# Kernel tuning notes

Measured on AMD Instinct MI355X. Metric: run time of the kernel, lower is better.

The kernel has to match this reference:

```python
import jax, jax.numpy as jnp
import numpy as np

N_NODES = 50000
N_EDGES = 600000
D = 128
N_GRAPHS = 64


def setup_inputs() -> dict:
    key = jax.random.key(0)
    ks = jax.random.split(key, 16)
    x = jax.random.normal(ks[0], (N_NODES, D), dtype=jnp.float32)
    edge_index = jax.random.randint(ks[1], (2, N_EDGES), 0, N_NODES, dtype=jnp.int64)
    batch = jnp.sort(jax.random.randint(ks[2], (N_NODES,), 0, N_GRAPHS, dtype=jnp.int64))
    s = 1.0 / np.sqrt(D)
    def lin(k, out_d, in_d):
        return jax.random.uniform(k, (out_d, in_d), jnp.float32, -s, s)
    inp = {"x": x, "edge_index": edge_index, "batch": batch}
    for i, base in zip(range(3), (3, 6, 9)):
        inp[f"W_rel{i+1}"] = lin(ks[base], D, D)
        inp[f"b_rel{i+1}"] = jax.random.uniform(ks[base + 1], (D,), jnp.float32, -s, s)
        inp[f"W_root{i+1}"] = lin(ks[base + 2], D, D)
    s5 = 1.0 / np.sqrt(5)
    inp["W1"] = lin(ks[12], 5, D)
    inp["b1"] = jax.random.uniform(ks[13], (5,), jnp.float32, -s, s)
    inp["W2"] = jax.random.uniform(ks[14], (1, 5), jnp.float32, -s5, s5)
    inp["b2"] = jax.random.uniform(ks[15], (1,), jnp.float32, -s5, s5)
    return inp


def graph_conv(x, src, dst, W_rel, b_rel, W_root):
    # PyG GraphConv: out_i = W_root x_i + W_rel * sum_{j->i} x_j + b_rel
    agg = jax.ops.segment_sum(x[src], dst, num_segments=N_NODES)  # [N, D]
    return agg @ W_rel.T + b_rel + x @ W_root.T


def reference(x, edge_index, batch,
              W_rel1, b_rel1, W_root1,
              W_rel2, b_rel2, W_root2,
              W_rel3, b_rel3, W_root3,
              W1, b1, W2, b2):
    src, dst = edge_index[0], edge_index[1]
    h = jax.nn.relu(graph_conv(x, src, dst, W_rel1, b_rel1, W_root1))
    h = jax.nn.relu(graph_conv(h, src, dst, W_rel2, b_rel2, W_root2))
    h = graph_conv(h, src, dst, W_rel3, b_rel3, W_root3)
    # global max pool over graphs
    g = jax.ops.segment_max(h, batch, num_segments=N_GRAPHS)  # [G, D]
    out = jax.nn.relu(g @ W1.T + b1) @ W2.T + b2  # [G, 1]
    return out
```

## Files before the change

kernel.cpp:

```cpp
#include <hip/hip_runtime.h>
#include <float.h>

#define N_NODES 50000
#define N_EDGES 600000
#define D 128
#define N_GRAPHS 64
#define SCAN_T 256
#define SCAN_NBLK ((N_NODES + SCAN_T - 1) / SCAN_T)

typedef __attribute__((ext_vector_type(8))) short short8;
typedef __attribute__((ext_vector_type(4))) float floatx4;

__device__ inline float bf2f(unsigned short h) {
    return __uint_as_float((unsigned)h << 16);
}
__device__ inline unsigned short f2bf(float f) {
    unsigned u = __float_as_uint(f);
    return (unsigned short)((u + 0x7fffu + ((u >> 16) & 1u)) >> 16);
}


__global__ void cast_prep(const float4* __restrict__ x,
                          ushort4* __restrict__ xb0, ushort4* __restrict__ xb1, int n4,
                          const float* __restrict__ Wr0, const float* __restrict__ Wo0,
                          const float* __restrict__ Wr1, const float* __restrict__ Wo1,
                          const float* __restrict__ Wr2, const float* __restrict__ Wo2,
                          unsigned short* __restrict__ B0, unsigned short* __restrict__ B1,
                          unsigned short* __restrict__ B2,
                          int* __restrict__ deg, float* __restrict__ g) {
    int idx = blockIdx.x * 256 + threadIdx.x;
    if (idx < N_NODES) deg[idx] = 0;
    if (idx < N_GRAPHS * D) g[idx] = -FLT_MAX;
    if (idx < n4) {
        float4 v = x[idx];
        ushort4 o;
        o.x = f2bf(v.x); o.y = f2bf(v.y); o.z = f2bf(v.z); o.w = f2bf(v.w);
        int node = idx >> 5;
        int q    = idx & 31;
        ushort4* dst = (q < 16) ? xb0 : xb1;
        dst[(size_t)node * 16 + (q & 15)] = o;
        return;
    }
    int w = idx - n4;
    if (w >= 3 * 128 * 256) return;
    int l = w >> 15;
    int r = w & 32767;
    int o = r >> 8, k = r & 255;
    const float* Wr = (l == 0) ? Wr0 : (l == 1) ? Wr1 : Wr2;
    const float* Wo = (l == 0) ? Wo0 : (l == 1) ? Wo1 : Wo2;
    unsigned short* B = (l == 0) ? B0 : (l == 1) ? B1 : B2;
    float v = (k < 128) ? Wr[o * 128 + k] : Wo[o * 128 + (k - 128)];
    B[r] = f2bf(v);
}


__global__ void count_deg(const int* __restrict__ ei, int* __restrict__ deg) {
    int e = blockIdx.x * 256 + threadIdx.x;
    if (e < N_EDGES) atomicAdd(&deg[ei[N_EDGES + e]], 1);
}

__global__ __launch_bounds__(SCAN_T) void block_sum(const int* __restrict__ deg,
                                                    int* __restrict__ blockSums) {
    __shared__ int s[SCAN_T];
    int tid = threadIdx.x;
    int i = blockIdx.x * SCAN_T + tid;
    s[tid] = (i < N_NODES) ? deg[i] : 0;
    __syncthreads();
    for (int off = SCAN_T / 2; off > 0; off >>= 1) {
        if (tid < off) s[tid] += s[tid + off];
        __syncthreads();
    }
    if (tid == 0) blockSums[blockIdx.x] = s[0];
}

__global__ __launch_bounds__(SCAN_T) void scan_write(const int* __restrict__ deg,
                                                     const int* __restrict__ blockSums,
                                                     int* __restrict__ row_start,
                                                     int* __restrict__ cursor) {
    __shared__ int bs[SCAN_T];
    __shared__ int s[SCAN_T];
    int tid = threadIdx.x;
    bs[tid] = (tid < SCAN_NBLK) ? blockSums[tid] : 0;
    __syncthreads();
    for (int off = 1; off < SCAN_T; off <<= 1) {
        int t = (tid >= off) ? bs[tid - off] : 0;
        __syncthreads();
        bs[tid] += t;
        __syncthreads();
    }
    int myOff = (blockIdx.x == 0) ? 0 : bs[blockIdx.x - 1];
    if (blockIdx.x == 0 && tid == SCAN_T - 1) row_start[N_NODES] = bs[tid];

    int i = blockIdx.x * SCAN_T + tid;
    int v = (i < N_NODES) ? deg[i] : 0;
    s[tid] = v;
    __syncthreads();
    for (int off = 1; off < SCAN_T; off <<= 1) {
        int t = (tid >= off) ? s[tid - off] : 0;
        __syncthreads();
        s[tid] += t;
        __syncthreads();
    }
    if (i < N_NODES) {
        int rs = myOff + s[tid] - v;
        row_start[i] = rs;
        cursor[i]    = rs;
    }
}

__global__ void fill_csr(const int* __restrict__ ei, int* __restrict__ cursor,
                         int* __restrict__ csr_src) {
    int e = blockIdx.x * 256 + threadIdx.x;
    if (e < N_EDGES) {
        int dst = ei[N_EDGES + e];
        int pos = atomicAdd(&cursor[dst], 1);
        csr_src[pos] = ei[e];
    }
}


#define ACC8(u) { a[0] += bf2f((unsigned short)(u)[0]); a[1] += bf2f((unsigned short)(u)[1]); \
                  a[2] += bf2f((unsigned short)(u)[2]); a[3] += bf2f((unsigned short)(u)[3]); \
                  a[4] += bf2f((unsigned short)(u)[4]); a[5] += bf2f((unsigned short)(u)[5]); \
                  a[6] += bf2f((unsigned short)(u)[6]); a[7] += bf2f((unsigned short)(u)[7]); }

__global__ __launch_bounds__(256) void gather_half(
    const unsigned short* __restrict__ xh,
    const int* __restrict__ row_start, const int* __restrict__ csr_src,
    unsigned short* __restrict__ aggh)
{
    int grp  = threadIdx.x >> 3;
    int ln   = threadIdx.x & 7;
    int node = blockIdx.x * 32 + grp;
    if (node >= N_NODES) return;
    int beg = row_start[node];
    int end = row_start[node + 1];

    float a[8];
#pragma unroll
    for (int i = 0; i < 8; ++i) a[i] = 0.f;

    for (int base = beg; base < end; base += 8) {
        int n = end - base; if (n > 8) n = 8;
        int idx = (ln < n) ? csr_src[base + ln] : 0;
        int j = 0;
        for (; j + 7 < n; j += 8) {
            int s0 = __shfl(idx, 0, 8); int s1 = __shfl(idx, 1, 8);
            int s2 = __shfl(idx, 2, 8); int s3 = __shfl(idx, 3, 8);
            int s4 = __shfl(idx, 4, 8); int s5 = __shfl(idx, 5, 8);
            int s6 = __shfl(idx, 6, 8); int s7 = __shfl(idx, 7, 8);
            short8 u0 = *(const short8*)(xh + (size_t)s0 * 64 + ln * 8);
            short8 u1 = *(const short8*)(xh + (size_t)s1 * 64 + ln * 8);
            short8 u2 = *(const short8*)(xh + (size_t)s2 * 64 + ln * 8);
            short8 u3 = *(const short8*)(xh + (size_t)s3 * 64 + ln * 8);
            short8 u4 = *(const short8*)(xh + (size_t)s4 * 64 + ln * 8);
            short8 u5 = *(const short8*)(xh + (size_t)s5 * 64 + ln * 8);
            short8 u6 = *(const short8*)(xh + (size_t)s6 * 64 + ln * 8);
            short8 u7 = *(const short8*)(xh + (size_t)s7 * 64 + ln * 8);
            ACC8(u0); ACC8(u1); ACC8(u2); ACC8(u3);
            ACC8(u4); ACC8(u5); ACC8(u6); ACC8(u7);
        }
        for (; j + 3 < n; j += 4) {
            int s0 = __shfl(idx, j,     8); int s1 = __shfl(idx, j + 1, 8);
            int s2 = __shfl(idx, j + 2, 8); int s3 = __shfl(idx, j + 3, 8);
            short8 u0 = *(const short8*)(xh + (size_t)s0 * 64 + ln * 8);
            short8 u1 = *(const short8*)(xh + (size_t)s1 * 64 + ln * 8);
            short8 u2 = *(const short8*)(xh + (size_t)s2 * 64 + ln * 8);
            short8 u3 = *(const short8*)(xh + (size_t)s3 * 64 + ln * 8);
            ACC8(u0); ACC8(u1); ACC8(u2); ACC8(u3);
        }
        for (; j < n; ++j) {
            int s0 = __shfl(idx, j, 8);
            short8 u0 = *(const short8*)(xh + (size_t)s0 * 64 + ln * 8);
            ACC8(u0);
        }
    }
    short8 r;
#pragma unroll
    for (int i = 0; i < 8; ++i) r[i] = (short)f2bf(a[i]);
    *(short8*)(aggh + (size_t)node * 64 + ln * 8) = r;
}


__device__ inline void stage_b_half(unsigned short* sB, const unsigned short* __restrict__ Bb,
                                    int tid, int h) {
#pragma unroll
    for (int i = 0; i < 8; ++i) {
        int flat = tid + i * 256;
        int fi = flat >> 6, ln = flat & 63;
        int mm = ln & 15, qq = ln >> 4;
        int ksL = fi >> 3, tt = fi & 7;
        short8 v = *(const short8*)(Bb + (size_t)(tt * 16 + mm) * 256
                                    + (h * 4 + ksL) * 32 + qq * 8);
        *(short8*)(sB + (size_t)flat * 8) = v;
    }
}


__global__ __launch_bounds__(256) void gemm_mfma(
    const unsigned short* __restrict__ agg0, const unsigned short* __restrict__ agg1,
    const unsigned short* __restrict__ x0,   const unsigned short* __restrict__ x1,
    const unsigned short* __restrict__ Bb, const float* __restrict__ bias,
    unsigned short* __restrict__ O0, unsigned short* __restrict__ O1, int relu)
{
    __shared__ unsigned short sB[16384];
    int tid  = threadIdx.x;
    int wave = tid >> 6;
    int lane = tid & 63;
    int m    = lane & 15;
    int quad = lane >> 4;
    int row0 = blockIdx.x * 64 + wave * 16;

    int arow = row0 + m;
    if (arow > N_NODES - 1) arow = N_NODES - 1;

    short8 af[8];
#pragma unroll
    for (int ks = 0; ks < 8; ++ks) {
        const unsigned short* Asrc =
            (ks < 2) ? agg0 : (ks < 4) ? agg1 : (ks < 6) ? x0 : x1;
        af[ks] = *(const short8*)(Asrc + (size_t)arow * 64 + (ks & 1) * 32 + quad * 8);
    }

    floatx4 acc[8];
#pragma unroll
    for (int t = 0; t < 8; ++t) acc[t] = (floatx4){0.f, 0.f, 0.f, 0.f};

    stage_b_half(sB, Bb, tid, 0);
    __syncthreads();
#pragma unroll
    for (int ksL = 0; ksL < 4; ++ksL)
#pragma unroll
        for (int t = 0; t < 8; ++t) {
            short8 b = *(const short8*)(sB + (size_t)((ksL * 8 + t) * 64 + lane) * 8);
            acc[t] = __builtin_amdgcn_mfma_f32_16x16x32_bf16(af[ksL], b, acc[t], 0, 0, 0);
        }
    __syncthreads();
    stage_b_half(sB, Bb, tid, 1);
    __syncthreads();
#pragma unroll
    for (int ksL = 0; ksL < 4; ++ksL)
#pragma unroll
        for (int t = 0; t < 8; ++t) {
            short8 b = *(const short8*)(sB + (size_t)((ksL * 8 + t) * 64 + lane) * 8);
            acc[t] = __builtin_amdgcn_mfma_f32_16x16x32_bf16(af[4 + ksL], b, acc[t], 0, 0, 0);
        }

#pragma unroll
    for (int t = 0; t < 8; ++t) {
        int col = t * 16 + m;
        float bv = bias[col];
        unsigned short* Oh = (t < 4) ? O0 : O1;
#pragma unroll
        for (int r = 0; r < 4; ++r) {
            int row = row0 + quad * 4 + r;
            if (row >= N_NODES) continue;
            float v = acc[t][r] + bv;
            if (relu) v = fmaxf(v, 0.f);
            Oh[(size_t)row * 64 + (col & 63)] = f2bf(v);
        }
    }
}


struct PoolShared {
    union {
        unsigned short b[16384];
        float c[64 * 129];
    };
};

__global__ __launch_bounds__(256) void gemm_pool(
    const unsigned short* __restrict__ agg0, const unsigned short* __restrict__ agg1,
    const unsigned short* __restrict__ x0,   const unsigned short* __restrict__ x1,
    const unsigned short* __restrict__ Bb, const float* __restrict__ bias,
    const int* __restrict__ batch, float* __restrict__ g)
{
    __shared__ PoolShared sh;
    __shared__ int bl[64];
    int tid  = threadIdx.x;
    int wave = tid >> 6;
    int lane = tid & 63;
    int m    = lane & 15;
    int quad = lane >> 4;
    int row0 = blockIdx.x * 64;

    int arow = row0 + wave * 16 + m;
    if (arow > N_NODES - 1) arow = N_NODES - 1;

    short8 af[8];
#pragma unroll
    for (int ks = 0; ks < 8; ++ks) {
        const unsigned short* Asrc =
            (ks < 2) ? agg0 : (ks < 4) ? agg1 : (ks < 6) ? x0 : x1;
        af[ks] = *(const short8*)(Asrc + (size_t)arow * 64 + (ks & 1) * 32 + quad * 8);
    }

    floatx4 acc[8];
#pragma unroll
    for (int t = 0; t < 8; ++t) acc[t] = (floatx4){0.f, 0.f, 0.f, 0.f};

    if (tid < 64) {
        int grow = row0 + tid;
        bl[tid] = (grow < N_NODES) ? batch[grow] : -1;
    }
    stage_b_half(sh.b, Bb, tid, 0);
    __syncthreads();
#pragma unroll
    for (int ksL = 0; ksL < 4; ++ksL)
#pragma unroll
        for (int t = 0; t < 8; ++t) {
            short8 b = *(const short8*)(sh.b + (size_t)((ksL * 8 + t) * 64 + lane) * 8);
            acc[t] = __builtin_amdgcn_mfma_f32_16x16x32_bf16(af[ksL], b, acc[t], 0, 0, 0);
        }
    __syncthreads();
    stage_b_half(sh.b, Bb, tid, 1);
    __syncthreads();
#pragma unroll
    for (int ksL = 0; ksL < 4; ++ksL)
#pragma unroll
        for (int t = 0; t < 8; ++t) {
            short8 b = *(const short8*)(sh.b + (size_t)((ksL * 8 + t) * 64 + lane) * 8);
            acc[t] = __builtin_amdgcn_mfma_f32_16x16x32_bf16(af[4 + ksL], b, acc[t], 0, 0, 0);
        }
    __syncthreads();

#pragma unroll
    for (int t = 0; t < 8; ++t) {
        int col = t * 16 + m;
        float bv = bias[col];
#pragma unroll
        for (int r = 0; r < 4; ++r)
            sh.c[(wave * 16 + quad * 4 + r) * 129 + col] = acc[t][r] + bv;
    }
    __syncthreads();

    int nvalid = min(64, N_NODES - row0);
    int b0 = bl[0], b1 = bl[nvalid - 1];
    int col  = tid & 127;
    int rbeg = (tid >> 7) * 32;
    for (int gg = b0; gg <= b1; ++gg) {
        float cur = -FLT_MAX;
#pragma unroll
        for (int r = 0; r < 32; ++r) {
            int rr = rbeg + r;
            float v = (bl[rr] == gg) ? sh.c[rr * 129 + col] : -FLT_MAX;
            cur = fmaxf(cur, v);
        }
        if (cur > -FLT_MAX) {
            float* ad = &g[gg * D + col];
            if (cur >= 0.f) atomicMax((int*)ad, __float_as_int(cur));
            else            atomicMin((unsigned int*)ad, __float_as_uint(cur));
        }
    }
}


__global__ __launch_bounds__(64) void mlp_head(const float* __restrict__ g,
                         const float* __restrict__ W1, const float* __restrict__ b1,
                         const float* __restrict__ W2, const float* __restrict__ b2,
                         float* __restrict__ out) {
    int gi = blockIdx.x;
    int lane = threadIdx.x;
    float x0 = g[gi * D + lane];
    float x1 = g[gi * D + 64 + lane];
    float o = b2[0];
#pragma unroll
    for (int j = 0; j < 5; ++j) {
        float p = x0 * W1[j * D + lane] + x1 * W1[j * D + 64 + lane];
#pragma unroll
        for (int off = 32; off > 0; off >>= 1) p += __shfl_xor(p, off, 64);
        o += fmaxf(p + b1[j], 0.f) * W2[j];
    }
    if (lane == 0) out[gi] = o;
}

extern "C" void kernel_launch(void* const* d_in, const int* in_sizes, int n_in,
                              void* d_out, int out_size, void* d_ws, size_t ws_size,
                              hipStream_t stream) {
    const float* x     = (const float*)d_in[0];
    const int*   ei    = (const int*)d_in[1];
    const int*   batch = (const int*)d_in[2];
    const float* Wrel[3]  = {(const float*)d_in[3], (const float*)d_in[6], (const float*)d_in[9]};
    const float* brel[3]  = {(const float*)d_in[4], (const float*)d_in[7], (const float*)d_in[10]};
    const float* Wroot[3] = {(const float*)d_in[5], (const float*)d_in[8], (const float*)d_in[11]};
    const float* W1 = (const float*)d_in[12];
    const float* b1 = (const float*)d_in[13];
    const float* W2 = (const float*)d_in[14];
    const float* b2 = (const float*)d_in[15];
    float* out = (float*)d_out;

    char* ws = (char*)d_ws;
    const size_t halfB = (size_t)N_NODES * 64 * sizeof(unsigned short);
    unsigned short* xb0  = (unsigned short*)(ws);
    unsigned short* xb1  = (unsigned short*)(ws + 1 * halfB);
    unsigned short* hb10 = (unsigned short*)(ws + 2 * halfB);
    unsigned short* hb11 = (unsigned short*)(ws + 3 * halfB);
    unsigned short* hb20 = (unsigned short*)(ws + 4 * halfB);
    unsigned short* hb21 = (unsigned short*)(ws + 5 * halfB);
    unsigned short* ag0  = (unsigned short*)(ws + 6 * halfB);
    unsigned short* ag1  = (unsigned short*)(ws + 7 * halfB);
    char* p = ws + 8 * halfB;
    unsigned short* Bb0 = (unsigned short*)p;   p += 128 * 256 * sizeof(unsigned short);
    unsigned short* Bb1 = (unsigned short*)p;   p += 128 * 256 * sizeof(unsigned short);
    unsigned short* Bb2 = (unsigned short*)p;   p += 128 * 256 * sizeof(unsigned short);
    float* g        = (float*)p;                p += N_GRAPHS * D * sizeof(float);
    int*   deg      = (int*)p;                  p += N_NODES * sizeof(int);
    int*   row_start= (int*)p;                  p += (N_NODES + 1) * sizeof(int);
    int*   cursor   = (int*)p;                  p += N_NODES * sizeof(int);
    int*   csr_src  = (int*)p;                  p += N_EDGES * sizeof(int);
    int*   blockSums= (int*)p;                  p += SCAN_NBLK * sizeof(int);

    const int n4 = N_NODES * D / 4;
    const int cast_total = n4 + 3 * 128 * 256;
    cast_prep<<<(cast_total + 255) / 256, 256, 0, stream>>>(
        (const float4*)x, (ushort4*)xb0, (ushort4*)xb1, n4,
        Wrel[0], Wroot[0], Wrel[1], Wroot[1], Wrel[2], Wroot[2],
        Bb0, Bb1, Bb2, deg, g);

    count_deg<<<(N_EDGES + 255) / 256, 256, 0, stream>>>(ei, deg);
    block_sum<<<SCAN_NBLK, SCAN_T, 0, stream>>>(deg, blockSums);
    scan_write<<<SCAN_NBLK, SCAN_T, 0, stream>>>(deg, blockSums, row_start, cursor);
    fill_csr<<<(N_EDGES + 255) / 256, 256, 0, stream>>>(ei, cursor, csr_src);

    const int ggrid = (N_NODES + 31) / 32;
    const int mgrid = (N_NODES + 63) / 64;

    gather_half<<<ggrid, 256, 0, stream>>>(xb0, row_start, csr_src, ag0);
    gather_half<<<ggrid, 256, 0, stream>>>(xb1, row_start, csr_src, ag1);
    gemm_mfma<<<mgrid, 256, 0, stream>>>(ag0, ag1, xb0, xb1, Bb0, brel[0], hb10, hb11, 1);
    gather_half<<<ggrid, 256, 0, stream>>>(hb10, row_start, csr_src, ag0);
    gather_half<<<ggrid, 256, 0, stream>>>(hb11, row_start, csr_src, ag1);
    gemm_mfma<<<mgrid, 256, 0, stream>>>(ag0, ag1, hb10, hb11, Bb1, brel[1], hb20, hb21, 1);
    gather_half<<<ggrid, 256, 0, stream>>>(hb20, row_start, csr_src, ag0);
    gather_half<<<ggrid, 256, 0, stream>>>(hb21, row_start, csr_src, ag1);
    gemm_pool<<<mgrid, 256, 0, stream>>>(ag0, ag1, hb20, hb21, Bb2, brel[2], batch, g);

    mlp_head<<<N_GRAPHS, 64, 0, stream>>>(g, W1, b1, W2, b2, out);
}
```

Baseline: 321.8 us.

## Quantize node features to int8 with per-node scale for neighbor gathers

After: 320.4 us. No clear change (-0.4%).

```diff
diff --git a/kernel.cpp b/kernel.cpp
--- a/kernel.cpp
+++ b/kernel.cpp
@@ -19,38 +19,79 @@
     return (unsigned short)((u + 0x7fffu + ((u >> 16) & 1u)) >> 16);
 }
 
-
-__global__ void cast_prep(const float4* __restrict__ x,
-                          ushort4* __restrict__ xb0, ushort4* __restrict__ xb1, int n4,
-                          const float* __restrict__ Wr0, const float* __restrict__ Wo0,
-                          const float* __restrict__ Wr1, const float* __restrict__ Wo1,
-                          const float* __restrict__ Wr2, const float* __restrict__ Wo2,
-                          unsigned short* __restrict__ B0, unsigned short* __restrict__ B1,
-                          unsigned short* __restrict__ B2,
-                          int* __restrict__ deg, float* __restrict__ g) {
-    int idx = blockIdx.x * 256 + threadIdx.x;
-    if (idx < N_NODES) deg[idx] = 0;
-    if (idx < N_GRAPHS * D) g[idx] = -FLT_MAX;
-    if (idx < n4) {
-        float4 v = x[idx];
-        ushort4 o;
-        o.x = f2bf(v.x); o.y = f2bf(v.y); o.z = f2bf(v.z); o.w = f2bf(v.w);
-        int node = idx >> 5;
-        int q    = idx & 31;
-        ushort4* dst = (q < 16) ? xb0 : xb1;
-        dst[(size_t)node * 16 + (q & 15)] = o;
+#define ACCQ(u, ss) {                                                            \
+    int w0_ = (u).x, w1_ = (u).y, w2_ = (u).z, w3_ = (u).w;                      \
+    a[ 0] += (float)(signed char)(w0_      ) * (ss);                             \
+    a[ 1] += (float)(signed char)(w0_ >>  8) * (ss);                             \
+    a[ 2] += (float)(signed char)(w0_ >> 16) * (ss);                             \
+    a[ 3] += (float)(w0_ >> 24)              * (ss);                             \
+    a[ 4] += (float)(signed char)(w1_      ) * (ss);                             \
+    a[ 5] += (float)(signed char)(w1_ >>  8) * (ss);                             \
+    a[ 6] += (float)(signed char)(w1_ >> 16) * (ss);                             \
+    a[ 7] += (float)(w1_ >> 24)              * (ss);                             \
+    a[ 8] += (float)(signed char)(w2_      ) * (ss);                             \
+    a[ 9] += (float)(signed char)(w2_ >>  8) * (ss);                             \
+    a[10] += (float)(signed char)(w2_ >> 16) * (ss);                             \
+    a[11] += (float)(w2_ >> 24)              * (ss);                             \
+    a[12] += (float)(signed char)(w3_      ) * (ss);                             \
+    a[13] += (float)(signed char)(w3_ >>  8) * (ss);                             \
+    a[14] += (float)(signed char)(w3_ >> 16) * (ss);                             \
+    a[15] += (float)(w3_ >> 24)              * (ss); }
+
+
+__global__ __launch_bounds__(256) void cast_prep(
+    const float* __restrict__ x,
+    unsigned short* __restrict__ xb, signed char* __restrict__ xq,
+    float* __restrict__ xs,
+    const float* __restrict__ Wr0, const float* __restrict__ Wo0,
+    const float* __restrict__ Wr1, const float* __restrict__ Wo1,
+    const float* __restrict__ Wr2, const float* __restrict__ Wo2,
+    unsigned short* __restrict__ B0, unsigned short* __restrict__ B1,
+    unsigned short* __restrict__ B2,
+    int* __restrict__ deg, float* __restrict__ g)
+{
+    int t = blockIdx.x * 256 + threadIdx.x;
+    if (t < N_NODES * 16) {
+        int node = t >> 4, ln = t & 15;
+        const float4* xr = (const float4*)(x + (size_t)node * D + ln * 8);
+        float4 v0 = xr[0], v1 = xr[1];
+        float v[8] = {v0.x, v0.y, v0.z, v0.w, v1.x, v1.y, v1.z, v1.w};
+        float am = 0.f;
+#pragma unroll
+        for (int i = 0; i < 8; ++i) am = fmaxf(am, fabsf(v[i]));
+#pragma unroll
+        for (int m = 1; m < 16; m <<= 1) am = fmaxf(am, __shfl_xor(am, m, 16));
+        float inv = (am > 0.f) ? 127.f / am : 0.f;
+        short8 hb;
+#pragma unroll
+        for (int i = 0; i < 8; ++i) hb[i] = (short)f2bf(v[i]);
+        *(short8*)(xb + (size_t)node * D + ln * 8) = hb;
+        int q0 = 0, q1 = 0;
+#pragma unroll
+        for (int i = 0; i < 4; ++i) { int q = (int)rintf(v[i]     * inv); q0 |= (q & 0xff) << (8 * i); }
+#pragma unroll
+        for (int i = 0; i < 4; ++i) { int q = (int)rintf(v[4 + i] * inv); q1 |= (q & 0xff) << (8 * i); }
+        int2 qp; qp.x = q0; qp.y = q1;
+        *(int2*)(xq + (size_t)node * D + ln * 8) = qp;
+        if (ln == 0) xs[node] = am * (1.f / 127.f);
         return;
     }
-    int w = idx - n4;
-    if (w >= 3 * 128 * 256) return;
-    int l = w >> 15;
-    int r = w & 32767;
-    int o = r >> 8, k = r & 255;
-    const float* Wr = (l == 0) ? Wr0 : (l == 1) ? Wr1 : Wr2;
-    const float* Wo = (l == 0) ? Wo0 : (l == 1) ? Wo1 : Wo2;
-    unsigned short* B = (l == 0) ? B0 : (l == 1) ? B1 : B2;
-    float v = (k < 128) ? Wr[o * 128 + k] : Wo[o * 128 + (k - 128)];
-    B[r] = f2bf(v);
+    int w = t - N_NODES * 16;
+    if (w < 3 * 128 * 256) {
+        int l = w >> 15;
+        int r = w & 32767;
+        int o = r >> 8, k = r & 255;
+        const float* Wr = (l == 0) ? Wr0 : (l == 1) ? Wr1 : Wr2;
+        const float* Wo = (l == 0) ? Wo0 : (l == 1) ? Wo1 : Wo2;
+        unsigned short* B = (l == 0) ? B0 : (l == 1) ? B1 : B2;
+        float v = (k < 128) ? Wr[o * 128 + k] : Wo[o * 128 + (k - 128)];
+        B[r] = f2bf(v);
+        return;
+    }
+    w -= 3 * 128 * 256;
+    if (w < N_NODES) { deg[w] = 0; return; }
+    w -= N_NODES;
+    if (w < N_GRAPHS * D) g[w] = -FLT_MAX;
 }
 
 
@@ -83,9 +124,9 @@
     bs[tid] = (tid < SCAN_NBLK) ? blockSums[tid] : 0;
     __syncthreads();
     for (int off = 1; off < SCAN_T; off <<= 1) {
-        int t = (tid >= off) ? bs[tid - off] : 0;
+        int tt = (tid >= off) ? bs[tid - off] : 0;
         __syncthreads();
-        bs[tid] += t;
+        bs[tid] += tt;
         __syncthreads();
     }
     int myOff = (blockIdx.x == 0) ? 0 : bs[blockIdx.x - 1];
@@ -96,9 +137,9 @@
     s[tid] = v;
     __syncthreads();
     for (int off = 1; off < SCAN_T; off <<= 1) {
-        int t = (tid >= off) ? s[tid - off] : 0;
+        int tt = (tid >= off) ? s[tid - off] : 0;
         __syncthreads();
-        s[tid] += t;
+        s[tid] += tt;
         __syncthreads();
     }
     if (i < N_NODES) {
@@ -119,15 +160,10 @@
 }
 
 
-#define ACC8(u) { a[0] += bf2f((unsigned short)(u)[0]); a[1] += bf2f((unsigned short)(u)[1]); \
-                  a[2] += bf2f((unsigned short)(u)[2]); a[3] += bf2f((unsigned short)(u)[3]); \
-                  a[4] += bf2f((unsigned short)(u)[4]); a[5] += bf2f((unsigned short)(u)[5]); \
-                  a[6] += bf2f((unsigned short)(u)[6]); a[7] += bf2f((unsigned short)(u)[7]); }
-
-__global__ __launch_bounds__(256) void gather_half(
-    const unsigned short* __restrict__ xh,
+__global__ __launch_bounds__(256) void gather_q(
+    const signed char* __restrict__ xq, const float* __restrict__ xs,
     const int* __restrict__ row_start, const int* __restrict__ csr_src,
-    unsigned short* __restrict__ aggh)
+    unsigned short* __restrict__ aggb)
 {
     int grp  = threadIdx.x >> 3;
     int ln   = threadIdx.x & 7;
@@ -136,49 +172,36 @@
     int beg = row_start[node];
     int end = row_start[node + 1];
 
-    float a[8];
-#pragma unroll
-    for (int i = 0; i < 8; ++i) a[i] = 0.f;
+    float a[16];
+#pragma unroll
+    for (int i = 0; i < 16; ++i) a[i] = 0.f;
 
     for (int base = beg; base < end; base += 8) {
         int n = end - base; if (n > 8) n = 8;
         int idx = (ln < n) ? csr_src[base + ln] : 0;
         int j = 0;
-        for (; j + 7 < n; j += 8) {
-            int s0 = __shfl(idx, 0, 8); int s1 = __shfl(idx, 1, 8);
-            int s2 = __shfl(idx, 2, 8); int s3 = __shfl(idx, 3, 8);
-            int s4 = __shfl(idx, 4, 8); int s5 = __shfl(idx, 5, 8);
-            int s6 = __shfl(idx, 6, 8); int s7 = __shfl(idx, 7, 8);
-            short8 u0 = *(const short8*)(xh + (size_t)s0 * 64 + ln * 8);
-            short8 u1 = *(const short8*)(xh + (size_t)s1 * 64 + ln * 8);
-            short8 u2 = *(const short8*)(xh + (size_t)s2 * 64 + ln * 8);
-            short8 u3 = *(const short8*)(xh + (size_t)s3 * 64 + ln * 8);
-            short8 u4 = *(const short8*)(xh + (size_t)s4 * 64 + ln * 8);
-            short8 u5 = *(const short8*)(xh + (size_t)s5 * 64 + ln * 8);
-            short8 u6 = *(const short8*)(xh + (size_t)s6 * 64 + ln * 8);
-            short8 u7 = *(const short8*)(xh + (size_t)s7 * 64 + ln * 8);
-            ACC8(u0); ACC8(u1); ACC8(u2); ACC8(u3);
-            ACC8(u4); ACC8(u5); ACC8(u6); ACC8(u7);
-        }
         for (; j + 3 < n; j += 4) {
             int s0 = __shfl(idx, j,     8); int s1 = __shfl(idx, j + 1, 8);
             int s2 = __shfl(idx, j + 2, 8); int s3 = __shfl(idx, j + 3, 8);
-            short8 u0 = *(const short8*)(xh + (size_t)s0 * 64 + ln * 8);
-            short8 u1 = *(const short8*)(xh + (size_t)s1 * 64 + ln * 8);
-            short8 u2 = *(const short8*)(xh + (size_t)s2 * 64 + ln * 8);
-            short8 u3 = *(const short8*)(xh + (size_t)s3 * 64 + ln * 8);
-            ACC8(u0); ACC8(u1); ACC8(u2); ACC8(u3);
+            int4 u0 = *(const int4*)(xq + (size_t)s0 * D + ln * 16);
+            int4 u1 = *(const int4*)(xq + (size_t)s1 * D + ln * 16);
+            int4 u2 = *(const int4*)(xq + (size_t)s2 * D + ln * 16);
+            int4 u3 = *(const int4*)(xq + (size_t)s3 * D + ln * 16);
+            float ss0 = xs[s0], ss1 = xs[s1], ss2 = xs[s2], ss3 = xs[s3];
+            ACCQ(u0, ss0); ACCQ(u1, ss1); ACCQ(u2, ss2); ACCQ(u3, ss3);
         }
         for (; j < n; ++j) {
             int s0 = __shfl(idx, j, 8);
-            short8 u0 = *(const short8*)(xh + (size_t)s0 * 64 + ln * 8);
-            ACC8(u0);
-        }
-    }
-    short8 r;
-#pragma unroll
-    for (int i = 0; i < 8; ++i) r[i] = (short)f2bf(a[i]);
-    *(short8*)(aggh + (size_t)node * 64 + ln * 8) = r;
+            int4 u0 = *(const int4*)(xq + (size_t)s0 * D + ln * 16);
+            float ss0 = xs[s0];
+            ACCQ(u0, ss0);
+        }
+    }
+    short8 r0, r1;
+#pragma unroll
+    for (int i = 0; i < 8; ++i) { r0[i] = (short)f2bf(a[i]); r1[i] = (short)f2bf(a[8 + i]); }
+    *(short8*)(aggb + (size_t)node * D + ln * 16)     = r0;
+    *(short8*)(aggb + (size_t)node * D + ln * 16 + 8) = r1;
 }
 
 
@@ -197,13 +220,20 @@
 }
 
 
+struct GemmShared {
+    union {
+        unsigned short b[16384];
+        float c[64 * 130];
+    };
+};
+
 __global__ __launch_bounds__(256) void gemm_mfma(
-    const unsigned short* __restrict__ agg0, const unsigned short* __restrict__ agg1,
-    const unsigned short* __restrict__ x0,   const unsigned short* __restrict__ x1,
+    const unsigned short* __restrict__ aggb, const unsigned short* __restrict__ xb,
     const unsigned short* __restrict__ Bb, const float* __restrict__ bias,
-    unsigned short* __restrict__ O0, unsigned short* __restrict__ O1, int relu)
+    unsigned short* __restrict__ Ob, signed char* __restrict__ Oq,
+    float* __restrict__ Os)
 {
-    __shared__ unsigned short sB[16384];
+    __shared__ GemmShared sh;
     int tid  = threadIdx.x;
     int wave = tid >> 6;
     int lane = tid & 63;
@@ -217,48 +247,83 @@
     short8 af[8];
 #pragma unroll
     for (int ks = 0; ks < 8; ++ks) {
-        const unsigned short* Asrc =
-            (ks < 2) ? agg0 : (ks < 4) ? agg1 : (ks < 6) ? x0 : x1;
-        af[ks] = *(const short8*)(Asrc + (size_t)arow * 64 + (ks & 1) * 32 + quad * 8);
+        const unsigned short* Asrc = (ks < 4) ? aggb : xb;
+        af[ks] = *(const short8*)(Asrc + (size_t)arow * 128 + (ks & 3) * 32 + quad * 8);
     }
 
     floatx4 acc[8];
 #pragma unroll
     for (int t = 0; t < 8; ++t) acc[t] = (floatx4){0.f, 0.f, 0.f, 0.f};
 
-    stage_b_half(sB, Bb, tid, 0);
+    stage_b_half(sh.b, Bb, tid, 0);
     __syncthreads();
 #pragma unroll
     for (int ksL = 0; ksL < 4; ++ksL)
 #pragma unroll
         for (int t = 0; t < 8; ++t) {
-            short8 b = *(const short8*)(sB + (size_t)((ksL * 8 + t) * 64 + lane) * 8);
+            short8 b = *(const short8*)(sh.b + (size_t)((ksL * 8 + t) * 64 + lane) * 8);
             acc[t] = __builtin_amdgcn_mfma_f32_16x16x32_bf16(af[ksL], b, acc[t], 0, 0, 0);
         }
     __syncthreads();
-    stage_b_half(sB, Bb, tid, 1);
+    stage_b_half(sh.b, Bb, tid, 1);
     __syncthreads();
 #pragma unroll
     for (int ksL = 0; ksL < 4; ++ksL)
 #pragma unroll
         for (int t = 0; t < 8; ++t) {
-            short8 b = *(const short8*)(sB + (size_t)((ksL * 8 + t) * 64 + lane) * 8);
+            short8 b = *(const short8*)(sh.b + (size_t)((ksL * 8 + t) * 64 + lane) * 8);
             acc[t] = __builtin_amdgcn_mfma_f32_16x16x32_bf16(af[4 + ksL], b, acc[t], 0, 0, 0);
         }
+    __syncthreads();
 
 #pragma unroll
     for (int t = 0; t < 8; ++t) {
         int col = t * 16 + m;
         float bv = bias[col];
-        unsigned short* Oh = (t < 4) ? O0 : O1;
 #pragma unroll
         for (int r = 0; r < 4; ++r) {
-            int row = row0 + quad * 4 + r;
-            if (row >= N_NODES) continue;
-            float v = acc[t][r] + bv;
-            if (relu) v = fmaxf(v, 0.f);
-            Oh[(size_t)row * 64 + (col & 63)] = f2bf(v);
-        }
+            float v = fmaxf(acc[t][r] + bv, 0.f);
+            sh.c[(wave * 16 + quad * 4 + r) * 130 + col] = v;
+        }
+    }
+    __syncthreads();
+
+    int lr  = tid >> 2;
+    int seg = tid & 3;
+    int grow = blockIdx.x * 64 + lr;
+    const float* cp = &sh.c[lr * 130 + seg * 32];
+    float vv[32];
+    float am = 0.f;
+#pragma unroll
+    for (int i = 0; i < 32; ++i) { vv[i] = cp[i]; am = fmaxf(am, fabsf(vv[i])); }
+    am = fmaxf(am, __shfl_xor(am, 1));
+    am = fmaxf(am, __shfl_xor(am, 2));
+    float inv = (am > 0.f) ? 127.f / am : 0.f;
+
+    if (grow < N_NODES) {
+#pragma unroll
+        for (int c8 = 0; c8 < 4; ++c8) {
+            short8 hb;
+#pragma unroll
+            for (int i = 0; i < 8; ++i) hb[i] = (short)f2bf(vv[c8 * 8 + i]);
+            *(short8*)(Ob + (size_t)grow * 128 + seg * 32 + c8 * 8) = hb;
+        }
+        int qd[8];
+#pragma unroll
+        for (int d = 0; d < 8; ++d) {
+            int q = 0;
+#pragma unroll
+            for (int i = 0; i < 4; ++i) {
+                int qq = (int)rintf(vv[d * 4 + i] * inv);
+                q |= (qq & 0xff) << (8 * i);
+            }
+            qd[d] = q;
+        }
+        int4 p0; p0.x = qd[0]; p0.y = qd[1]; p0.z = qd[2]; p0.w = qd[3];
+        int4 p1; p1.x = qd[4]; p1.y = qd[5]; p1.z = qd[6]; p1.w = qd[7];
+        *(int4*)(Oq + (size_t)grow * 128 + seg * 32)      = p0;
+        *(int4*)(Oq + (size_t)grow * 128 + seg * 32 + 16) = p1;
+        if (seg == 0) Os[grow] = am * (1.f / 127.f);
     }
 }
 
@@ -271,8 +336,7 @@
 };
 
 __global__ __launch_bounds__(256) void gemm_pool(
-    const unsigned short* __restrict__ agg0, const unsigned short* __restrict__ agg1,
-    const unsigned short* __restrict__ x0,   const unsigned short* __restrict__ x1,
+    const unsigned short* __restrict__ aggb, const unsigned short* __restrict__ xb,
     const unsigned short* __restrict__ Bb, const float* __restrict__ bias,
     const int* __restrict__ batch, float* __restrict__ g)
 {
@@ -291,9 +355,8 @@
     short8 af[8];
 #pragma unroll
     for (int ks = 0; ks < 8; ++ks) {
-        const unsigned short* Asrc =
-            (ks < 2) ? agg0 : (ks < 4) ? agg1 : (ks < 6) ? x0 : x1;
-        af[ks] = *(const short8*)(Asrc + (size_t)arow * 64 + (ks & 1) * 32 + quad * 8);
+        const unsigned short* Asrc = (ks < 4) ? aggb : xb;
+        af[ks] = *(const short8*)(Asrc + (size_t)arow * 128 + (ks & 3) * 32 + quad * 8);
     }
 
     floatx4 acc[8];
@@ -391,16 +454,19 @@
     float* out = (float*)d_out;
 
     char* ws = (char*)d_ws;
-    const size_t halfB = (size_t)N_NODES * 64 * sizeof(unsigned short);
-    unsigned short* xb0  = (unsigned short*)(ws);
-    unsigned short* xb1  = (unsigned short*)(ws + 1 * halfB);
-    unsigned short* hb10 = (unsigned short*)(ws + 2 * halfB);
-    unsigned short* hb11 = (unsigned short*)(ws + 3 * halfB);
-    unsigned short* hb20 = (unsigned short*)(ws + 4 * halfB);
-    unsigned short* hb21 = (unsigned short*)(ws + 5 * halfB);
-    unsigned short* ag0  = (unsigned short*)(ws + 6 * halfB);
-    unsigned short* ag1  = (unsigned short*)(ws + 7 * halfB);
-    char* p = ws + 8 * halfB;
+    const size_t nodeB16 = (size_t)N_NODES * D * sizeof(unsigned short);
+    const size_t nodeB8  = (size_t)N_NODES * D;
+    unsigned short* xb   = (unsigned short*)(ws);
+    unsigned short* h1b  = (unsigned short*)(ws + 1 * nodeB16);
+    unsigned short* h2b  = (unsigned short*)(ws + 2 * nodeB16);
+    unsigned short* aggb = (unsigned short*)(ws + 3 * nodeB16);
+    char* p = ws + 4 * nodeB16;
+    signed char* xq  = (signed char*)p;  p += nodeB8;
+    signed char* h1q = (signed char*)p;  p += nodeB8;
+    signed char* h2q = (signed char*)p;  p += nodeB8;
+    float* xs  = (float*)p;  p += N_NODES * sizeof(float);
+    float* h1s = (float*)p;  p += N_NODES * sizeof(float);
+    float* h2s = (float*)p;  p += N_NODES * sizeof(float);
     unsigned short* Bb0 = (unsigned short*)p;   p += 128 * 256 * sizeof(unsigned short);
     unsigned short* Bb1 = (unsigned short*)p;   p += 128 * 256 * sizeof(unsigned short);
     unsigned short* Bb2 = (unsigned short*)p;   p += 128 * 256 * sizeof(unsigned short);
@@ -411,10 +477,9 @@
     int*   csr_src  = (int*)p;                  p += N_EDGES * sizeof(int);
     int*   blockSums= (int*)p;                  p += SCAN_NBLK * sizeof(int);
 
-    const int n4 = N_NODES * D / 4;
-    const int cast_total = n4 + 3 * 128 * 256;
+    const int cast_total = N_NODES * 16 + 3 * 128 * 256 + N_NODES + N_GRAPHS * D;
     cast_prep<<<(cast_total + 255) / 256, 256, 0, stream>>>(
-        (const float4*)x, (ushort4*)xb0, (ushort4*)xb1, n4,
+        x, xb, xq, xs,
         Wrel[0], Wroot[0], Wrel[1], Wroot[1], Wrel[2], Wroot[2],
         Bb0, Bb1, Bb2, deg, g);
 
@@ -426,15 +491,12 @@
     const int ggrid = (N_NODES + 31) / 32;
     const int mgrid = (N_NODES + 63) / 64;
 
-    gather_half<<<ggrid, 256, 0, stream>>>(xb0, row_start, csr_src, ag0);
-    gather_half<<<ggrid, 256, 0, stream>>>(xb1, row_start, csr_src, ag1);
-    gemm_mfma<<<mgrid, 256, 0, stream>>>(ag0, ag1, xb0, xb1, Bb0, brel[0], hb10, hb11, 1);
-    gather_half<<<ggrid, 256, 0, stream>>>(hb10, row_start, csr_src, ag0);
-    gather_half<<<ggrid, 256, 0, stream>>>(hb11, row_start, csr_src, ag1);
-    gemm_mfma<<<mgrid, 256, 0, stream>>>(ag0, ag1, hb10, hb11, Bb1, brel[1], hb20, hb21, 1);
-    gather_half<<<ggrid, 256, 0, stream>>>(hb20, row_start, csr_src, ag0);
-    gather_half<<<ggrid, 256, 0, stream>>>(hb21, row_start, csr_src, ag1);
-    gemm_pool<<<mgrid, 256, 0, stream>>>(ag0, ag1, hb20, hb21, Bb2, brel[2], batch, g);
+    gather_q<<<ggrid, 256, 0, stream>>>(xq, xs, row_start, csr_src, aggb);
+    gemm_mfma<<<mgrid, 256, 0, stream>>>(aggb, xb, Bb0, brel[0], h1b, h1q, h1s);
+    gather_q<<<ggrid, 256, 0, stream>>>(h1q, h1s, row_start, csr_src, aggb);
+    gemm_mfma<<<mgrid, 256, 0, stream>>>(aggb, h1b, Bb1, brel[1], h2b, h2q, h2s);
+    gather_q<<<ggrid, 256, 0, stream>>>(h2q, h2s, row_start, csr_src, aggb);
+    gemm_pool<<<mgrid, 256, 0, stream>>>(aggb, h2b, Bb2, brel[2], batch, g);
 
     mlp_head<<<N_GRAPHS, 64, 0, stream>>>(g, W1, b1, W2, b2, out);
 }
```
